# Optimization experiments

Hardware: AMD Instinct MI355X
Metric: run time of the kernel (lower is better)

The kernel has to match this reference:

```python
import jax, jax.numpy as jnp
import numpy as np

B, N, D, K, CF = 2, 4096, 128, 32, 16
EI = 2 * D + 1  # edge_input_dim = 257 (edge_feat=0, fourier_feat=0)


def setup_inputs() -> dict:
    key = jax.random.key(0)
    ks = jax.random.split(key, 10)
    rn = lambda k, shp, s=0.05: jax.random.normal(k, shp, jnp.float32) * s
    return {
        "h": rn(ks[0], (B, N, D), 1.0),
        "x": rn(ks[1], (B, N, 3), 1.0),
        "mask": jnp.ones((B, N), dtype=bool),
        # edge_mlp: Linear(EI, 2EI) -> SiLU -> Linear(2EI, CF) -> SiLU
        "We1": rn(ks[2], (EI, 2 * EI)), "be1": jnp.zeros((2 * EI,), jnp.float32),
        "We2": rn(ks[3], (2 * EI, CF)), "be2": jnp.zeros((CF,), jnp.float32),
        # coors_mlp: Linear(CF, 4CF) -> SiLU -> Linear(4CF, 1)
        "Wc1": rn(ks[4], (CF, 4 * CF)), "bc1": jnp.zeros((4 * CF,), jnp.float32),
        "Wc2": rn(ks[5], (4 * CF, 1)), "bc2": jnp.zeros((1,), jnp.float32),
        # node_mlp: Linear(D+CF, 2D) -> SiLU -> Linear(2D, D)
        "Wn1": rn(ks[6], (D + CF, 2 * D)), "bn1": jnp.zeros((2 * D,), jnp.float32),
        "Wn2": rn(ks[7], (2 * D, D)), "bn2": jnp.zeros((D,), jnp.float32),
    }


def _forward(h, x, mask, We1, be1, We2, be2, Wc1, bc1, Wc2, bc2, Wn1, bn1, Wn2, bn2):
    silu = jax.nn.silu
    b, n, d = h.shape
    # pairwise relative coordinates and squared distances
    rel = x[:, :, None, :] - x[:, None, :, :]            # [b, n, n, 3]
    dist = jnp.sum(rel * rel, axis=-1)                   # [b, n, n]
    # top-K nearest neighbors (smallest distance)
    _, idx = jax.lax.top_k(-dist, K)                     # [b, n, K]
    rel_k = jnp.take_along_axis(rel, idx[..., None], axis=2)   # [b, n, K, 3]
    dist_k = jnp.take_along_axis(dist, idx, axis=2)[..., None]  # [b, n, K, 1]
    bidx = jnp.arange(b)[:, None, None]
    feats_j = h[bidx, idx]                               # [b, n, K, d]
    feats_i = jnp.broadcast_to(h[:, :, None, :], (b, n, K, d))
    edge_in = jnp.concatenate([feats_i, feats_j, dist_k], axis=-1)  # [b, n, K, 2d+1]
    # edge MLP
    m_ij = silu(silu(edge_in @ We1 + be1) @ We2 + be2)   # [b, n, K, CF]
    # coordinate weights
    cw = (silu(m_ij @ Wc1 + bc1) @ Wc2 + bc2)[..., 0]    # [b, n, K]
    mask_ij = mask[:, :, None] & mask[bidx, idx]         # [b, n, K]
    cw = jnp.where(mask_ij, cw, 0.0)
    coors_out = jnp.einsum('bij,bijc->bic', cw, rel_k) + x
    # node update
    m_i = m_ij.sum(axis=-2)                              # [b, n, CF]
    node_in = jnp.concatenate([h, m_i], axis=-1)
    node_out = silu(node_in @ Wn1 + bn1) @ Wn2 + bn2 + h
    return node_out, coors_out


def reference(h, x, mask, We1, be1, We2, be2, Wc1, bc1, Wc2, bc2, Wn1, bn1, Wn2, bn2):
    return _forward(h, x, mask, We1, be1, We2, be2, Wc1, bc1, Wc2, bc2, Wn1, bn1, Wn2, bn2)
```

## Files before the change

kernel.cpp:

```cpp
#include <hip/hip_runtime.h>
#include <hip/hip_bf16.h>

#define BB    2
#define NNODE 4096
#define DD    128
#define KK    32
#define CFX   16

typedef __attribute__((ext_vector_type(8))) short bf16x8;
typedef __attribute__((ext_vector_type(4))) float f32x4;

__device__ __forceinline__ unsigned short f2bf(float f) {
    __hip_bfloat16 h = __float2bfloat16(f);
    return *reinterpret_cast<unsigned short*>(&h);
}
__device__ __forceinline__ unsigned pk2(float lo, float hi) {
    __hip_bfloat162 v = __float22bfloat162_rn(make_float2(lo, hi));
    return *reinterpret_cast<unsigned*>(&v);
}
__device__ __forceinline__ float silu_f(float v) {
    float e = __expf(-v);
    return v * __builtin_amdgcn_rcpf(1.f + e);
}
__device__ __forceinline__ float dist3(float xi0, float xi1, float xi2,
                                       const float* __restrict__ xb, int j) {
    float d0 = __fsub_rn(xi0, xb[3 * j]);
    float d1 = __fsub_rn(xi1, xb[3 * j + 1]);
    float d2 = __fsub_rn(xi2, xb[3 * j + 2]);
    return __fadd_rn(__fadd_rn(__fmul_rn(d0, d0), __fmul_rn(d1, d1)), __fmul_rn(d2, d2));
}

__global__ void prep_kernel(const float* __restrict__ We1, const float* __restrict__ We2,
                            const float* __restrict__ Wn1, const float* __restrict__ Wn2,
                            unsigned short* __restrict__ W1pack, unsigned short* __restrict__ W2p2,
                            unsigned short* __restrict__ Wn1p, unsigned short* __restrict__ Wn2p) {
    int tid = blockIdx.x * 256 + threadIdx.x;
    int stride = gridDim.x * 256;
    for (int p = tid; p < 9 * 36 * 64 * 8; p += stride) {
        int i = p & 7, lane = (p >> 3) & 63, rest = p >> 9;
        int nb = rest % 36, ks = rest / 36;
        int n = nb * 16 + (lane & 15);
        int k = ks * 32 + 8 * (lane >> 4) + i;
        W1pack[p] = (k < 257 && n < 514) ? f2bf(We1[k * 514 + n]) : (unsigned short)0;
    }
    for (int p = tid; p < 4 * 5 * 64 * 8; p += stride) {
        int i = p & 7, lane = (p >> 3) & 63, rest = p >> 9;
        int ks2 = rest % 5, wn = rest / 5;
        int g = lane >> 4, f = lane & 15;
        int nloc = ks2 * 32 + 16 * (i >> 2) + 4 * g + (i & 3);
        int ng = wn * 144 + nloc;
        W2p2[p] = (nloc < 144 && ng < 514) ? f2bf(We2[ng * 16 + f]) : (unsigned short)0;
    }
    for (int p = tid; p < 5 * 16 * 64 * 8; p += stride) {
        int i = p & 7, lane = (p >> 3) & 63, rest = p >> 9;
        int nb = rest % 16, ks = rest / 16;
        int u = nb * 16 + (lane & 15);
        int k = ks * 32 + 8 * (lane >> 4) + i;
        Wn1p[p] = (k < 144) ? f2bf(Wn1[k * 256 + u]) : (unsigned short)0;
    }
    for (int p = tid; p < 8 * 8 * 64 * 8; p += stride) {
        int i = p & 7, lane = (p >> 3) & 63, rest = p >> 9;
        int nb = rest % 8, ks = rest / 8;
        int d = nb * 16 + (lane & 15);
        int k = ks * 32 + 8 * (lane >> 4) + i;
        Wn2p[p] = f2bf(Wn2[k * 128 + d]);
    }
}

__global__ __launch_bounds__(256) void pre_kernel(
    const float* __restrict__ h, const float* __restrict__ be1,
    const unsigned short* __restrict__ W1pack, float* __restrict__ pre_g)
{
    __shared__ unsigned short nin[16][136];
    const int t = threadIdx.x;
    const int gn0 = blockIdx.x * 16;
    const int wn = t >> 6, lane = t & 63;
    const int l15 = lane & 15, g = lane >> 4;

    for (int q = t; q < 16 * 32; q += 256) {
        int node = q >> 5, c4 = q & 31;
        float4 v = *(const float4*)(h + (size_t)(gn0 + node) * DD + c4 * 4);
        *(uint2*)&nin[node][c4 * 4] = make_uint2(pk2(v.x, v.y), pk2(v.z, v.w));
    }
    __syncthreads();

    const bf16x8* W1v = (const bf16x8*)W1pack;
    f32x4 acc[9];
    #pragma unroll
    for (int nb = 0; nb < 9; ++nb)
        #pragma unroll
        for (int r = 0; r < 4; ++r) acc[nb][r] = 0.f;
    #pragma unroll
    for (int ks = 0; ks < 4; ++ks) {
        bf16x8 bfr = *(const bf16x8*)&nin[l15][ks * 32 + 8 * g];
        #pragma unroll
        for (int nb = 0; nb < 9; ++nb) {
            bf16x8 af = W1v[((size_t)(ks * 36 + wn * 9 + nb)) * 64 + lane];
            acc[nb] = __builtin_amdgcn_mfma_f32_16x16x32_bf16(af, bfr, acc[nb], 0, 0, 0);
        }
    }
    float* outp = pre_g + (size_t)(gn0 + l15) * 576;
    #pragma unroll
    for (int nb = 0; nb < 9; ++nb) {
        int n0 = wn * 144 + nb * 16 + 4 * g;
        float4 o;
        o.x = acc[nb][0] + ((n0 + 0) < 514 ? be1[n0 + 0] : 0.f);
        o.y = acc[nb][1] + ((n0 + 1) < 514 ? be1[n0 + 1] : 0.f);
        o.z = acc[nb][2] + ((n0 + 2) < 514 ? be1[n0 + 2] : 0.f);
        o.w = acc[nb][3] + ((n0 + 3) < 514 ? be1[n0 + 3] : 0.f);
        *(float4*)(outp + n0) = o;
    }
}

#define EQCAP 36
#define CANDCAP 1024
__global__ __launch_bounds__(256) void knn_kernel(const float* __restrict__ x,
                                                  int* __restrict__ idx_o,
                                                  float* __restrict__ relk_o,
                                                  float* __restrict__ distk_o) {
    __shared__ unsigned hist[4][256];
    __shared__ unsigned wsum[4];
    __shared__ unsigned sel[2];
    __shared__ unsigned shA, shB;
    __shared__ int out_j[KK];
    __shared__ int eqbuf[EQCAP];
    __shared__ uint2 cand[CANDCAP];

    const int t = threadIdx.x;
    const int ln = t & 63, wv = t >> 6;
    const int gn = blockIdx.x;
    const int b = gn >> 12, i = gn & 4095;
    const float* xb = x + (size_t)b * NNODE * 3;
    const float xi0 = xb[3 * i], xi1 = xb[3 * i + 1], xi2 = xb[3 * i + 2];

    #pragma unroll
    for (int q2 = 0; q2 < 4; ++q2) hist[q2][t] = 0;
    __syncthreads();

    unsigned ub[16];
    #pragma unroll
    for (int s = 0; s < 16; ++s) {
        float d = dist3(xi0, xi1, xi2, xb, t + 256 * s);
        ub[s] = __float_as_uint(d);
        atomicAdd(&hist[wv][ub[s] >> 24], 1u);
    }
    __syncthreads();

    int kk = KK;
    {
        unsigned hv = hist[0][t] + hist[1][t] + hist[2][t] + hist[3][t];
        unsigned v = hv;
        #pragma unroll
        for (int off = 1; off < 64; off <<= 1) {
            unsigned o = __shfl_up(v, off, 64);
            if (ln >= off) v += o;
        }
        if (ln == 63) wsum[wv] = v;
        __syncthreads();
        unsigned add = 0;
        #pragma unroll
        for (int w = 0; w < 4; ++w) add += (w < wv) ? wsum[w] : 0u;
        unsigned incl = v + add, excl = incl - hv;
        if ((unsigned)kk > excl && (unsigned)kk <= incl) { sel[0] = (unsigned)t; sel[1] = (unsigned)kk - excl; }
        __syncthreads();
    }
    unsigned prefix = sel[0];
    kk = (int)sel[1];
    __syncthreads();

    unsigned pc = 0;
    #pragma unroll
    for (int s = 0; s < 16; ++s) {
        unsigned tb = ub[s] >> 24;
        pc += (tb < prefix) ? 0x10000u : (tb == prefix ? 1u : 0u);
    }
    {
        unsigned v = pc;
        #pragma unroll
        for (int off = 1; off < 64; off <<= 1) {
            unsigned o = __shfl_up(v, off, 64);
            if (ln >= off) v += o;
        }
        if (ln == 63) wsum[wv] = v;
        __syncthreads();
        unsigned add = 0;
        #pragma unroll
        for (int w = 0; w < 4; ++w) add += (w < wv) ? wsum[w] : 0u;
        unsigned incl = v + add, excl = incl - pc;
        if (t == 255) { shA = incl >> 16; shB = incl & 0xFFFFu; }
        __syncthreads();
        unsigned wl = excl >> 16, wc = excl & 0xFFFFu;
        #pragma unroll
        for (int s = 0; s < 16; ++s) {
            unsigned u = ub[s];
            unsigned tb = u >> 24;
            int j = t + 256 * s;
            if (tb < prefix) { out_j[wl++] = j; }
            else if (tb == prefix) { if (wc < CANDCAP) cand[wc] = make_uint2(u, (unsigned)j); ++wc; }
        }
    }
    __syncthreads();
    const unsigned totL0 = shA, totC = shB;
    const bool fullscan = (totC > CANDCAP);

    for (int r = 1; r < 4; ++r) {
        const int sh = 24 - 8 * r;
        #pragma unroll
        for (int q2 = 0; q2 < 4; ++q2) hist[q2][t] = 0;
        __syncthreads();
        if (!fullscan) {
            for (int ii = t; ii < (int)totC; ii += 256) {
                unsigned u = cand[ii].x;
                if ((u >> (sh + 8)) == prefix) atomicAdd(&hist[wv][(u >> sh) & 255], 1u);
            }
        } else {
            #pragma unroll
            for (int s = 0; s < 16; ++s) {
                unsigned u = ub[s];
                if ((u >> (sh + 8)) == prefix) atomicAdd(&hist[wv][(u >> sh) & 255], 1u);
            }
        }
        __syncthreads();
        unsigned hv = hist[0][t] + hist[1][t] + hist[2][t] + hist[3][t];
        unsigned v = hv;
        #pragma unroll
        for (int off = 1; off < 64; off <<= 1) {
            unsigned o = __shfl_up(v, off, 64);
            if (ln >= off) v += o;
        }
        if (ln == 63) wsum[wv] = v;
        __syncthreads();
        unsigned add = 0;
        #pragma unroll
        for (int w = 0; w < 4; ++w) add += (w < wv) ? wsum[w] : 0u;
        unsigned incl = v + add, excl = incl - hv;
        if ((unsigned)kk > excl && (unsigned)kk <= incl) { sel[0] = (unsigned)t; sel[1] = (unsigned)kk - excl; }
        __syncthreads();
        prefix = (prefix << 8) | sel[0];
        kk = (int)sel[1];
        __syncthreads();
    }
    const unsigned T = prefix;

    int totL;
    if (!fullscan) {
        unsigned pc2 = 0;
        for (int ii = t; ii < (int)totC; ii += 256) {
            unsigned u = cand[ii].x;
            pc2 += (u < T) ? 0x10000u : (u == T ? 1u : 0u);
        }
        unsigned v = pc2;
        #pragma unroll
        for (int off = 1; off < 64; off <<= 1) {
            unsigned o = __shfl_up(v, off, 64);
            if (ln >= off) v += o;
        }
        if (ln == 63) wsum[wv] = v;
        __syncthreads();
        unsigned add = 0;
        #pragma unroll
        for (int w = 0; w < 4; ++w) add += (w < wv) ? wsum[w] : 0u;
        unsigned incl = v + add, excl = incl - pc2;
        if (t == 255) { shA = incl >> 16; shB = incl & 0xFFFFu; }
        __syncthreads();
        unsigned w2 = totL0 + (excl >> 16), we = excl & 0xFFFFu;
        for (int ii = t; ii < (int)totC; ii += 256) {
            unsigned u = cand[ii].x;
            int j = (int)cand[ii].y;
            if (u < T) { out_j[w2++] = j; }
            else if (u == T) { if (we < EQCAP) eqbuf[we] = j; ++we; }
        }
        __syncthreads();
        totL = (int)(totL0 + shA);
        const unsigned totE = shB;
        if (t == 0) {
            int need = KK - totL;
            if (totE <= EQCAP) {
                for (int a = 1; a < (int)totE; ++a) {
                    int key = eqbuf[a], c = a - 1;
                    while (c >= 0 && eqbuf[c] > key) { eqbuf[c + 1] = eqbuf[c]; --c; }
                    eqbuf[c + 1] = key;
                }
                for (int q = 0; q < need; ++q) out_j[totL + q] = eqbuf[q];
            } else {
                int taken = 0;
                for (int j = 0; j < NNODE && taken < need; ++j)
                    if (__float_as_uint(dist3(xi0, xi1, xi2, xb, j)) == T) out_j[totL + taken++] = j;
            }
        }
    } else {
        unsigned pc2 = 0;
        #pragma unroll
        for (int s = 0; s < 16; ++s) {
            unsigned u = ub[s];
            pc2 += (u < T) ? 0x10000u : (u == T ? 1u : 0u);
        }
        unsigned v = pc2;
        #pragma unroll
        for (int off = 1; off < 64; off <<= 1) {
            unsigned o = __shfl_up(v, off, 64);
            if (ln >= off) v += o;
        }
        if (ln == 63) wsum[wv] = v;
        __syncthreads();
        unsigned add = 0;
        #pragma unroll
        for (int w = 0; w < 4; ++w) add += (w < wv) ? wsum[w] : 0u;
        unsigned incl = v + add, excl = incl - pc2;
        if (t == 255) { shA = incl >> 16; shB = incl & 0xFFFFu; }
        __syncthreads();
        unsigned w2 = excl >> 16, we = excl & 0xFFFFu;
        #pragma unroll
        for (int s = 0; s < 16; ++s) {
            unsigned u = ub[s];
            int j = t + 256 * s;
            if (u < T) { out_j[w2++] = j; }
            else if (u == T) { if (we < EQCAP) eqbuf[we] = j; ++we; }
        }
        __syncthreads();
        totL = (int)shA;
        const unsigned totE = shB;
        if (t == 0) {
            int need = KK - totL;
            if (totE <= EQCAP) {
                for (int a = 1; a < (int)totE; ++a) {
                    int key = eqbuf[a], c = a - 1;
                    while (c >= 0 && eqbuf[c] > key) { eqbuf[c + 1] = eqbuf[c]; --c; }
                    eqbuf[c + 1] = key;
                }
                for (int q = 0; q < need; ++q) out_j[totL + q] = eqbuf[q];
            } else {
                int taken = 0;
                for (int j = 0; j < NNODE && taken < need; ++j)
                    if (__float_as_uint(dist3(xi0, xi1, xi2, xb, j)) == T) out_j[totL + taken++] = j;
            }
        }
    }
    __syncthreads();

    if (t < KK) {
        int j = out_j[t];
        size_t eo = (size_t)gn * KK + t;
        idx_o[eo] = j;
        float r0 = __fsub_rn(xi0, xb[3 * j]);
        float r1 = __fsub_rn(xi1, xb[3 * j + 1]);
        float r2 = __fsub_rn(xi2, xb[3 * j + 2]);
        relk_o[eo * 3 + 0] = r0;
        relk_o[eo * 3 + 1] = r1;
        relk_o[eo * 3 + 2] = r2;
        distk_o[eo] = __fadd_rn(__fadd_rn(__fmul_rn(r0, r0), __fmul_rn(r1, r1)), __fmul_rn(r2, r2));
    }
}

__global__ __launch_bounds__(256, 2) void edge_kernel(
    const float* __restrict__ h, const float* __restrict__ x, const int* __restrict__ mask,
    const float* __restrict__ be2,
    const float* __restrict__ Wc1, const float* __restrict__ bc1,
    const float* __restrict__ Wc2, const float* __restrict__ bc2,
    const int* __restrict__ idx, const float* __restrict__ relk, const float* __restrict__ distk,
    const unsigned short* __restrict__ W1pack, const unsigned short* __restrict__ W2p2,
    const float* __restrict__ pre_g,
    float* __restrict__ m_i_out, float* __restrict__ coors_out)
{
    __shared__ unsigned short E2[64][168];
    __shared__ float pre_s[2 * 576];
    __shared__ int   j_s[64];
    __shared__ float cw_s[64];
    __shared__ float m_s4[4 * 64 * 16];
    __shared__ float m_sF[64 * 17];

    const int t = threadIdx.x;
    const int gn0 = blockIdx.x * 2;
    const int b = gn0 >> 12;
    const int wn = t >> 6, lane = t & 63;
    const int l15 = lane & 15, g = lane >> 4;

    if (t < 64) {
        size_t eo = (size_t)gn0 * KK + t;
        j_s[t] = idx[eo];
        float dv = distk[eo];
        ushort2* p = (ushort2*)&E2[t][128];
        p[0] = make_ushort2(f2bf(dv), 0);
        #pragma unroll
        for (int z = 1; z < 20; ++z) p[z] = make_ushort2(0, 0);
    }
    {
        const float4* src = (const float4*)(pre_g + (size_t)gn0 * 576);
        float4* dst = (float4*)pre_s;
        for (int i2 = t; i2 < 288; i2 += 256) dst[i2] = src[i2];
    }
    __syncthreads();

    for (int q = t; q < 64 * 32; q += 256) {
        int e = q >> 5, d4 = q & 31;
        int j = j_s[e];
        float4 v = *(const float4*)(h + ((size_t)b * NNODE + j) * DD + d4 * 4);
        *(uint2*)&E2[e][d4 * 4] = make_uint2(pk2(v.x, v.y), pk2(v.z, v.w));
    }
    __syncthreads();

    const bf16x8* W1v = (const bf16x8*)W1pack;
    const bf16x8* W2v = (const bf16x8*)W2p2;
    int erow[4];
    #pragma unroll
    for (int et = 0; et < 4; ++et) erow[et] = et * 16 + l15;

    f32x4 acc2[4];
    #pragma unroll
    for (int et = 0; et < 4; ++et)
        #pragma unroll
        for (int r = 0; r < 4; ++r) acc2[et][r] = 0.f;

    #pragma unroll
    for (int c = 0; c < 2; ++c) {
        f32x4 acc[4][4];
        #pragma unroll
        for (int nb = 0; nb < 4; ++nb)
            #pragma unroll
            for (int et = 0; et < 4; ++et)
                acc[nb][et] = *(const f32x4*)&pre_s[(et >> 1) * 576 + wn * 144 + (c * 4 + nb) * 16 + 4 * g];
        #pragma unroll
        for (int ks = 0; ks < 5; ++ks) {
            const bf16x8* wp = W1v + ((size_t)((ks + 4) * 36 + wn * 9 + c * 4)) * 64 + lane;
            bf16x8 afr[4];
            #pragma unroll
            for (int nb = 0; nb < 4; ++nb) afr[nb] = wp[nb * 64];
            bf16x8 bfr[4];
            #pragma unroll
            for (int et = 0; et < 4; ++et)
                bfr[et] = *(const bf16x8*)&E2[erow[et]][ks * 32 + 8 * g];
            #pragma unroll
            for (int nb = 0; nb < 4; ++nb)
                #pragma unroll
                for (int et = 0; et < 4; ++et)
                    acc[nb][et] = __builtin_amdgcn_mfma_f32_16x16x32_bf16(afr[nb], bfr[et], acc[nb][et], 0, 0, 0);
        }
        #pragma unroll
        for (int nb = 0; nb < 4; ++nb)
            #pragma unroll
            for (int et = 0; et < 4; ++et)
                #pragma unroll
                for (int r = 0; r < 4; ++r)
                    acc[nb][et][r] = silu_f(acc[nb][et][r]);
        #pragma unroll
        for (int qq = 0; qq < 2; ++qq) {
            int ks2 = 2 * c + qq;
            bf16x8 a2 = W2v[(size_t)(wn * 5 + ks2) * 64 + lane];
            #pragma unroll
            for (int et = 0; et < 4; ++et) {
                union { unsigned u[4]; bf16x8 v; } cv;
                cv.u[0] = pk2(acc[2 * qq][et][0], acc[2 * qq][et][1]);
                cv.u[1] = pk2(acc[2 * qq][et][2], acc[2 * qq][et][3]);
                cv.u[2] = pk2(acc[2 * qq + 1][et][0], acc[2 * qq + 1][et][1]);
                cv.u[3] = pk2(acc[2 * qq + 1][et][2], acc[2 * qq + 1][et][3]);
                acc2[et] = __builtin_amdgcn_mfma_f32_16x16x32_bf16(a2, cv.v, acc2[et], 0, 0, 0);
            }
        }
    }
    {
        f32x4 acc8[4];
        #pragma unroll
        for (int et = 0; et < 4; ++et)
            acc8[et] = *(const f32x4*)&pre_s[(et >> 1) * 576 + wn * 144 + 128 + 4 * g];
        #pragma unroll
        for (int ks = 0; ks < 5; ++ks) {
            bf16x8 af = W1v[((size_t)((ks + 4) * 36 + wn * 9 + 8)) * 64 + lane];
            bf16x8 bfr[4];
            #pragma unroll
            for (int et = 0; et < 4; ++et)
                bfr[et] = *(const bf16x8*)&E2[erow[et]][ks * 32 + 8 * g];
            #pragma unroll
            for (int et = 0; et < 4; ++et)
                acc8[et] = __builtin_amdgcn_mfma_f32_16x16x32_bf16(af, bfr[et], acc8[et], 0, 0, 0);
        }
        #pragma unroll
        for (int et = 0; et < 4; ++et)
            #pragma unroll
            for (int r = 0; r < 4; ++r)
                acc8[et][r] = silu_f(acc8[et][r]);
        bf16x8 a2 = W2v[(size_t)(wn * 5 + 4) * 64 + lane];
        #pragma unroll
        for (int et = 0; et < 4; ++et) {
            union { unsigned u[4]; bf16x8 v; } cv;
            cv.u[0] = pk2(acc8[et][0], acc8[et][1]);
            cv.u[1] = pk2(acc8[et][2], acc8[et][3]);
            cv.u[2] = 0; cv.u[3] = 0;
            acc2[et] = __builtin_amdgcn_mfma_f32_16x16x32_bf16(a2, cv.v, acc2[et], 0, 0, 0);
        }
    }
    #pragma unroll
    for (int et = 0; et < 4; ++et)
        *(f32x4*)&m_s4[((wn * 64) + erow[et]) * 16 + 4 * g] = acc2[et];
    __syncthreads();

    #pragma unroll
    for (int i2 = t; i2 < 64 * 16; i2 += 256) {
        int e = i2 >> 4, f = i2 & 15;
        float s = m_s4[e * 16 + f] + m_s4[(64 + e) * 16 + f]
                + m_s4[(128 + e) * 16 + f] + m_s4[(192 + e) * 16 + f];
        m_sF[e * 17 + f] = silu_f(s + be2[f]);
    }
    __syncthreads();

    {
        const int ee = t >> 2, q4 = t & 3;
        const int u0 = q4 * 16;
        float mm[16];
        #pragma unroll
        for (int f = 0; f < 16; ++f) mm[f] = m_sF[ee * 17 + f];
        float h2[16];
        {
            const float4* bp = (const float4*)(bc1 + u0);
            float4 b0 = bp[0], b1 = bp[1], b2v = bp[2], b3 = bp[3];
            h2[0]=b0.x; h2[1]=b0.y; h2[2]=b0.z; h2[3]=b0.w;
            h2[4]=b1.x; h2[5]=b1.y; h2[6]=b1.z; h2[7]=b1.w;
            h2[8]=b2v.x; h2[9]=b2v.y; h2[10]=b2v.z; h2[11]=b2v.w;
            h2[12]=b3.x; h2[13]=b3.y; h2[14]=b3.z; h2[15]=b3.w;
        }
        #pragma unroll
        for (int f = 0; f < 16; ++f) {
            const float4* wp = (const float4*)(Wc1 + (size_t)f * 64 + u0);
            float4 w0 = wp[0], w1 = wp[1], w2 = wp[2], w3 = wp[3];
            float v = mm[f];
            h2[0]  = fmaf(v, w0.x, h2[0]);  h2[1]  = fmaf(v, w0.y, h2[1]);
            h2[2]  = fmaf(v, w0.z, h2[2]);  h2[3]  = fmaf(v, w0.w, h2[3]);
            h2[4]  = fmaf(v, w1.x, h2[4]);  h2[5]  = fmaf(v, w1.y, h2[5]);
            h2[6]  = fmaf(v, w1.z, h2[6]);  h2[7]  = fmaf(v, w1.w, h2[7]);
            h2[8]  = fmaf(v, w2.x, h2[8]);  h2[9]  = fmaf(v, w2.y, h2[9]);
            h2[10] = fmaf(v, w2.z, h2[10]); h2[11] = fmaf(v, w2.w, h2[11]);
            h2[12] = fmaf(v, w3.x, h2[12]); h2[13] = fmaf(v, w3.y, h2[13]);
            h2[14] = fmaf(v, w3.z, h2[14]); h2[15] = fmaf(v, w3.w, h2[15]);
        }
        float cw = 0.f;
        const float4* cp = (const float4*)(Wc2 + u0);
        float4 c0 = cp[0], c1 = cp[1], c2 = cp[2], c3 = cp[3];
        const float wv[16] = {c0.x,c0.y,c0.z,c0.w, c1.x,c1.y,c1.z,c1.w,
                              c2.x,c2.y,c2.z,c2.w, c3.x,c3.y,c3.z,c3.w};
        #pragma unroll
        for (int r = 0; r < 16; ++r) cw = fmaf(silu_f(h2[r]), wv[r], cw);
        cw += __shfl_xor(cw, 1, 64);
        cw += __shfl_xor(cw, 2, 64);
        if (q4 == 0) {
            cw += bc2[0];
            int gnode = gn0 + (ee >> 5);
            int mi = mask[gnode];
            int mj = mask[b * NNODE + j_s[ee]];
            cw_s[ee] = (mi != 0 && mj != 0) ? cw : 0.f;
        }
    }
    __syncthreads();

    if (t < 32) {
        int n = t >> 4, f = t & 15;
        float s = 0.f;
        #pragma unroll
        for (int k2 = 0; k2 < 32; ++k2) s += m_sF[(n * 32 + k2) * 17 + f];
        m_i_out[(size_t)(gn0 + n) * CFX + f] = s;
    } else if (t < 38) {
        int r = t - 32;
        int n = r / 3, c = r - n * 3;
        const float* rp = relk + ((size_t)gn0 * KK + n * 32) * 3 + c;
        float s = 0.f;
        #pragma unroll
        for (int k2 = 0; k2 < 32; ++k2) s = fmaf(cw_s[n * 32 + k2], rp[k2 * 3], s);
        coors_out[(size_t)(gn0 + n) * 3 + c] = s + x[(size_t)(gn0 + n) * 3 + c];
    }
}

__global__ __launch_bounds__(256) void node_kernel(
    const float* __restrict__ h, const float* __restrict__ m_i,
    const unsigned short* __restrict__ Wn1p, const float* __restrict__ bn1,
    const unsigned short* __restrict__ Wn2p, const float* __restrict__ bn2,
    float* __restrict__ node_out)
{
    __shared__ unsigned short nin[32][168];
    __shared__ unsigned short hid[32][264];

    const int t = threadIdx.x;
    const int gn0 = blockIdx.x * 32;
    const int wn = t >> 6, lane = t & 63;
    const int l15 = lane & 15, g = lane >> 4;

    for (int q = t; q < 32 * 32; q += 256) {
        int node = q >> 5, c4 = q & 31;
        float4 v = *(const float4*)(h + (size_t)(gn0 + node) * DD + c4 * 4);
        *(uint2*)&nin[node][c4 * 4] = make_uint2(pk2(v.x, v.y), pk2(v.z, v.w));
    }
    if (t < 128) {
        int node = t >> 2, c4 = t & 3;
        float4 v = *(const float4*)(m_i + (size_t)(gn0 + node) * CFX + c4 * 4);
        *(uint2*)&nin[node][128 + c4 * 4] = make_uint2(pk2(v.x, v.y), pk2(v.z, v.w));
    } else if (t < 224) {
        int r = t - 128;
        int node = r / 3, cc = (r - node * 3) * 8;
        *(uint4*)&nin[node][144 + cc] = make_uint4(0, 0, 0, 0);
    }
    __syncthreads();

    const bf16x8* A1 = (const bf16x8*)Wn1p;
    f32x4 acc[4][2];
    #pragma unroll
    for (int nb = 0; nb < 4; ++nb)
        #pragma unroll
        for (int et = 0; et < 2; ++et)
            #pragma unroll
            for (int r = 0; r < 4; ++r) acc[nb][et][r] = 0.f;
    #pragma unroll
    for (int ks = 0; ks < 5; ++ks) {
        const bf16x8* wp = A1 + ((size_t)(ks * 16 + wn * 4)) * 64 + lane;
        bf16x8 afr[4];
        #pragma unroll
        for (int nb = 0; nb < 4; ++nb) afr[nb] = wp[nb * 64];
        bf16x8 b0 = *(const bf16x8*)&nin[l15][ks * 32 + 8 * g];
        bf16x8 b1 = *(const bf16x8*)&nin[16 + l15][ks * 32 + 8 * g];
        #pragma unroll
        for (int nb = 0; nb < 4; ++nb) {
            acc[nb][0] = __builtin_amdgcn_mfma_f32_16x16x32_bf16(afr[nb], b0, acc[nb][0], 0, 0, 0);
            acc[nb][1] = __builtin_amdgcn_mfma_f32_16x16x32_bf16(afr[nb], b1, acc[nb][1], 0, 0, 0);
        }
    }
    #pragma unroll
    for (int nb = 0; nb < 4; ++nb) {
        int u0 = (wn * 4 + nb) * 16 + 4 * g;
        f32x4 bv = *(const f32x4*)&bn1[u0];
        #pragma unroll
        for (int et = 0; et < 2; ++et) {
            float s0 = silu_f(acc[nb][et][0] + bv[0]);
            float s1 = silu_f(acc[nb][et][1] + bv[1]);
            float s2 = silu_f(acc[nb][et][2] + bv[2]);
            float s3 = silu_f(acc[nb][et][3] + bv[3]);
            *(uint2*)&hid[et * 16 + l15][u0] = make_uint2(pk2(s0, s1), pk2(s2, s3));
        }
    }
    __syncthreads();

    const bf16x8* A2 = (const bf16x8*)Wn2p;
    f32x4 acc2[2][2];
    #pragma unroll
    for (int nb = 0; nb < 2; ++nb)
        #pragma unroll
        for (int et = 0; et < 2; ++et)
            #pragma unroll
            for (int r = 0; r < 4; ++r) acc2[nb][et][r] = 0.f;
    #pragma unroll
    for (int ks = 0; ks < 8; ++ks) {
        const bf16x8* wp = A2 + ((size_t)(ks * 8 + wn * 2)) * 64 + lane;
        bf16x8 a0 = wp[0], a1 = wp[64];
        bf16x8 b0 = *(const bf16x8*)&hid[l15][ks * 32 + 8 * g];
        bf16x8 b1 = *(const bf16x8*)&hid[16 + l15][ks * 32 + 8 * g];
        acc2[0][0] = __builtin_amdgcn_mfma_f32_16x16x32_bf16(a0, b0, acc2[0][0], 0, 0, 0);
        acc2[0][1] = __builtin_amdgcn_mfma_f32_16x16x32_bf16(a0, b1, acc2[0][1], 0, 0, 0);
        acc2[1][0] = __builtin_amdgcn_mfma_f32_16x16x32_bf16(a1, b0, acc2[1][0], 0, 0, 0);
        acc2[1][1] = __builtin_amdgcn_mfma_f32_16x16x32_bf16(a1, b1, acc2[1][1], 0, 0, 0);
    }
    #pragma unroll
    for (int nb = 0; nb < 2; ++nb) {
        int d0 = (wn * 2 + nb) * 16 + 4 * g;
        f32x4 bv = *(const f32x4*)&bn2[d0];
        #pragma unroll
        for (int et = 0; et < 2; ++et) {
            int gnode = gn0 + et * 16 + l15;
            float4 hv = *(const float4*)(h + (size_t)gnode * DD + d0);
            float4 o;
            o.x = acc2[nb][et][0] + bv[0] + hv.x;
            o.y = acc2[nb][et][1] + bv[1] + hv.y;
            o.z = acc2[nb][et][2] + bv[2] + hv.z;
            o.w = acc2[nb][et][3] + bv[3] + hv.w;
            *(float4*)(node_out + (size_t)gnode * DD + d0) = o;
        }
    }
}

extern "C" void kernel_launch(void* const* d_in, const int* in_sizes, int n_in,
                              void* d_out, int out_size, void* d_ws, size_t ws_size,
                              hipStream_t stream) {
    const float* h   = (const float*)d_in[0];
    const float* x   = (const float*)d_in[1];
    const int*   mask= (const int*)d_in[2];
    const float* We1 = (const float*)d_in[3];
    const float* be1 = (const float*)d_in[4];
    const float* We2 = (const float*)d_in[5];
    const float* be2 = (const float*)d_in[6];
    const float* Wc1 = (const float*)d_in[7];
    const float* bc1 = (const float*)d_in[8];
    const float* Wc2 = (const float*)d_in[9];
    const float* bc2 = (const float*)d_in[10];
    const float* Wn1 = (const float*)d_in[11];
    const float* bn1 = (const float*)d_in[12];
    const float* Wn2 = (const float*)d_in[13];
    const float* bn2 = (const float*)d_in[14];

    float* node_out  = (float*)d_out;
    float* coors_out = node_out + (size_t)BB * NNODE * DD;

    char* ws = (char*)d_ws;
    int*   idx    = (int*)ws;            ws += (size_t)BB * NNODE * KK * 4;
    float* relk   = (float*)ws;          ws += (size_t)BB * NNODE * KK * 3 * 4;
    float* distk  = (float*)ws;          ws += (size_t)BB * NNODE * KK * 4;
    float* m_i    = (float*)ws;          ws += (size_t)BB * NNODE * CFX * 4;
    unsigned short* W1pack = (unsigned short*)ws;  ws += (size_t)9 * 36 * 64 * 8 * 2;
    unsigned short* W2p2   = (unsigned short*)ws;  ws += (size_t)4 * 5 * 64 * 8 * 2;
    unsigned short* Wn1p   = (unsigned short*)ws;  ws += (size_t)5 * 16 * 64 * 8 * 2;
    unsigned short* Wn2p   = (unsigned short*)ws;  ws += (size_t)8 * 8 * 64 * 8 * 2;
    float* pre_g  = (float*)ws;          ws += (size_t)BB * NNODE * 576 * 4;

    prep_kernel<<<256, 256, 0, stream>>>(We1, We2, Wn1, Wn2, W1pack, W2p2, Wn1p, Wn2p);
    pre_kernel<<<BB * NNODE / 16, 256, 0, stream>>>(h, be1, W1pack, pre_g);
    knn_kernel<<<BB * NNODE, 256, 0, stream>>>(x, idx, relk, distk);
    edge_kernel<<<BB * NNODE / 2, 256, 0, stream>>>(h, x, mask, be2, Wc1, bc1, Wc2, bc2,
                                                    idx, relk, distk, W1pack, W2p2, pre_g,
                                                    m_i, coors_out);
    node_kernel<<<BB * NNODE / 32, 256, 0, stream>>>(h, m_i, Wn1p, bn1, Wn2p, bn2, node_out);
}
```

Before: 288.0 us.

## Precompute per-node neighbor projection of first edge layer, gather instead of MMA

```diff
diff --git a/kernel.cpp b/kernel.cpp
--- a/kernel.cpp
+++ b/kernel.cpp
@@ -69,7 +69,8 @@
 
 __global__ __launch_bounds__(256) void pre_kernel(
     const float* __restrict__ h, const float* __restrict__ be1,
-    const unsigned short* __restrict__ W1pack, float* __restrict__ pre_g)
+    const unsigned short* __restrict__ W1pack,
+    float* __restrict__ preI_g, unsigned short* __restrict__ preJ_g)
 {
     __shared__ unsigned short nin[16][136];
     const int t = threadIdx.x;
@@ -85,30 +86,54 @@
     __syncthreads();
 
     const bf16x8* W1v = (const bf16x8*)W1pack;
-    f32x4 acc[9];
-    #pragma unroll
-    for (int nb = 0; nb < 9; ++nb)
-        #pragma unroll
-        for (int r = 0; r < 4; ++r) acc[nb][r] = 0.f;
-    #pragma unroll
-    for (int ks = 0; ks < 4; ++ks) {
-        bf16x8 bfr = *(const bf16x8*)&nin[l15][ks * 32 + 8 * g];
+    {
+        f32x4 acc[9];
+        #pragma unroll
+        for (int nb = 0; nb < 9; ++nb)
+            #pragma unroll
+            for (int r = 0; r < 4; ++r) acc[nb][r] = 0.f;
+        #pragma unroll
+        for (int ks = 0; ks < 4; ++ks) {
+            bf16x8 bfr = *(const bf16x8*)&nin[l15][ks * 32 + 8 * g];
+            #pragma unroll
+            for (int nb = 0; nb < 9; ++nb) {
+                bf16x8 af = W1v[((size_t)(ks * 36 + wn * 9 + nb)) * 64 + lane];
+                acc[nb] = __builtin_amdgcn_mfma_f32_16x16x32_bf16(af, bfr, acc[nb], 0, 0, 0);
+            }
+        }
+        float* outp = preI_g + (size_t)(gn0 + l15) * 576;
         #pragma unroll
         for (int nb = 0; nb < 9; ++nb) {
-            bf16x8 af = W1v[((size_t)(ks * 36 + wn * 9 + nb)) * 64 + lane];
-            acc[nb] = __builtin_amdgcn_mfma_f32_16x16x32_bf16(af, bfr, acc[nb], 0, 0, 0);
-        }
-    }
-    float* outp = pre_g + (size_t)(gn0 + l15) * 576;
-    #pragma unroll
-    for (int nb = 0; nb < 9; ++nb) {
-        int n0 = wn * 144 + nb * 16 + 4 * g;
-        float4 o;
-        o.x = acc[nb][0] + ((n0 + 0) < 514 ? be1[n0 + 0] : 0.f);
-        o.y = acc[nb][1] + ((n0 + 1) < 514 ? be1[n0 + 1] : 0.f);
-        o.z = acc[nb][2] + ((n0 + 2) < 514 ? be1[n0 + 2] : 0.f);
-        o.w = acc[nb][3] + ((n0 + 3) < 514 ? be1[n0 + 3] : 0.f);
-        *(float4*)(outp + n0) = o;
+            int n0 = wn * 144 + nb * 16 + 4 * g;
+            float4 o;
+            o.x = acc[nb][0] + ((n0 + 0) < 514 ? be1[n0 + 0] : 0.f);
+            o.y = acc[nb][1] + ((n0 + 1) < 514 ? be1[n0 + 1] : 0.f);
+            o.z = acc[nb][2] + ((n0 + 2) < 514 ? be1[n0 + 2] : 0.f);
+            o.w = acc[nb][3] + ((n0 + 3) < 514 ? be1[n0 + 3] : 0.f);
+            *(float4*)(outp + n0) = o;
+        }
+    }
+    {
+        f32x4 acc[9];
+        #pragma unroll
+        for (int nb = 0; nb < 9; ++nb)
+            #pragma unroll
+            for (int r = 0; r < 4; ++r) acc[nb][r] = 0.f;
+        #pragma unroll
+        for (int ks = 0; ks < 4; ++ks) {
+            bf16x8 bfr = *(const bf16x8*)&nin[l15][ks * 32 + 8 * g];
+            #pragma unroll
+            for (int nb = 0; nb < 9; ++nb) {
+                bf16x8 af = W1v[((size_t)((ks + 4) * 36 + wn * 9 + nb)) * 64 + lane];
+                acc[nb] = __builtin_amdgcn_mfma_f32_16x16x32_bf16(af, bfr, acc[nb], 0, 0, 0);
+            }
+        }
+        unsigned short* outp = preJ_g + (size_t)(gn0 + l15) * 576;
+        #pragma unroll
+        for (int nb = 0; nb < 9; ++nb) {
+            int n0 = wn * 144 + nb * 16 + 4 * g;
+            *(uint2*)(outp + n0) = make_uint2(pk2(acc[nb][0], acc[nb][1]), pk2(acc[nb][2], acc[nb][3]));
+        }
     }
 }
 
@@ -352,19 +377,20 @@
     }
 }
 
-__global__ __launch_bounds__(256, 2) void edge_kernel(
-    const float* __restrict__ h, const float* __restrict__ x, const int* __restrict__ mask,
-    const float* __restrict__ be2,
+__global__ __launch_bounds__(256) void edge_kernel(
+    const float* __restrict__ x, const int* __restrict__ mask,
+    const float* __restrict__ We1, const float* __restrict__ be2,
     const float* __restrict__ Wc1, const float* __restrict__ bc1,
     const float* __restrict__ Wc2, const float* __restrict__ bc2,
     const int* __restrict__ idx, const float* __restrict__ relk, const float* __restrict__ distk,
-    const unsigned short* __restrict__ W1pack, const unsigned short* __restrict__ W2p2,
-    const float* __restrict__ pre_g,
+    const unsigned short* __restrict__ W2p2,
+    const float* __restrict__ preI_g, const unsigned short* __restrict__ preJ_g,
     float* __restrict__ m_i_out, float* __restrict__ coors_out)
 {
-    __shared__ unsigned short E2[64][168];
     __shared__ float pre_s[2 * 576];
+    __shared__ float wd_s[576];
     __shared__ int   j_s[64];
+    __shared__ float dist_s[64];
     __shared__ float cw_s[64];
     __shared__ float m_s4[4 * 64 * 16];
     __shared__ float m_sF[64 * 17];
@@ -378,32 +404,26 @@
     if (t < 64) {
         size_t eo = (size_t)gn0 * KK + t;
         j_s[t] = idx[eo];
-        float dv = distk[eo];
-        ushort2* p = (ushort2*)&E2[t][128];
-        p[0] = make_ushort2(f2bf(dv), 0);
-        #pragma unroll
-        for (int z = 1; z < 20; ++z) p[z] = make_ushort2(0, 0);
-    }
+        dist_s[t] = distk[eo];
+    }
+    for (int i2 = t; i2 < 576; i2 += 256) wd_s[i2] = (i2 < 514) ? We1[256 * 514 + i2] : 0.f;
     {
-        const float4* src = (const float4*)(pre_g + (size_t)gn0 * 576);
+        const float4* src = (const float4*)(preI_g + (size_t)gn0 * 576);
         float4* dst = (float4*)pre_s;
         for (int i2 = t; i2 < 288; i2 += 256) dst[i2] = src[i2];
     }
     __syncthreads();
 
-    for (int q = t; q < 64 * 32; q += 256) {
-        int e = q >> 5, d4 = q & 31;
-        int j = j_s[e];
-        float4 v = *(const float4*)(h + ((size_t)b * NNODE + j) * DD + d4 * 4);
-        *(uint2*)&E2[e][d4 * 4] = make_uint2(pk2(v.x, v.y), pk2(v.z, v.w));
-    }
-    __syncthreads();
-
-    const bf16x8* W1v = (const bf16x8*)W1pack;
     const bf16x8* W2v = (const bf16x8*)W2p2;
     int erow[4];
-    #pragma unroll
-    for (int et = 0; et < 4; ++et) erow[et] = et * 16 + l15;
+    size_t jrow[4];
+    float de[4];
+    #pragma unroll
+    for (int et = 0; et < 4; ++et) {
+        erow[et] = et * 16 + l15;
+        jrow[et] = ((size_t)b * NNODE + j_s[erow[et]]) * 576;
+        de[et] = dist_s[erow[et]];
+    }
 
     f32x4 acc2[4];
     #pragma unroll
@@ -415,33 +435,23 @@
     for (int c = 0; c < 2; ++c) {
         f32x4 acc[4][4];
         #pragma unroll
-        for (int nb = 0; nb < 4; ++nb)
-            #pragma unroll
-            for (int et = 0; et < 4; ++et)
-                acc[nb][et] = *(const f32x4*)&pre_s[(et >> 1) * 576 + wn * 144 + (c * 4 + nb) * 16 + 4 * g];
-        #pragma unroll
-        for (int ks = 0; ks < 5; ++ks) {
-            const bf16x8* wp = W1v + ((size_t)((ks + 4) * 36 + wn * 9 + c * 4)) * 64 + lane;
-            bf16x8 afr[4];
-            #pragma unroll
-            for (int nb = 0; nb < 4; ++nb) afr[nb] = wp[nb * 64];
-            bf16x8 bfr[4];
-            #pragma unroll
-            for (int et = 0; et < 4; ++et)
-                bfr[et] = *(const bf16x8*)&E2[erow[et]][ks * 32 + 8 * g];
-            #pragma unroll
-            for (int nb = 0; nb < 4; ++nb)
-                #pragma unroll
-                for (int et = 0; et < 4; ++et)
-                    acc[nb][et] = __builtin_amdgcn_mfma_f32_16x16x32_bf16(afr[nb], bfr[et], acc[nb][et], 0, 0, 0);
-        }
-        #pragma unroll
-        for (int nb = 0; nb < 4; ++nb)
-            #pragma unroll
-            for (int et = 0; et < 4; ++et)
-                #pragma unroll
-                for (int r = 0; r < 4; ++r)
-                    acc[nb][et][r] = silu_f(acc[nb][et][r]);
+        for (int nb = 0; nb < 4; ++nb) {
+            const int n0 = wn * 144 + (c * 4 + nb) * 16 + 4 * g;
+            f32x4 wdv = *(const f32x4*)&wd_s[n0];
+            #pragma unroll
+            for (int et = 0; et < 4; ++et) {
+                f32x4 pi = *(const f32x4*)&pre_s[(et >> 1) * 576 + n0];
+                uint2 pj = *(const uint2*)(preJ_g + jrow[et] + n0);
+                float p0 = __uint_as_float(pj.x << 16);
+                float p1 = __uint_as_float(pj.x & 0xFFFF0000u);
+                float p2 = __uint_as_float(pj.y << 16);
+                float p3 = __uint_as_float(pj.y & 0xFFFF0000u);
+                acc[nb][et][0] = silu_f(pi[0] + p0 + de[et] * wdv[0]);
+                acc[nb][et][1] = silu_f(pi[1] + p1 + de[et] * wdv[1]);
+                acc[nb][et][2] = silu_f(pi[2] + p2 + de[et] * wdv[2]);
+                acc[nb][et][3] = silu_f(pi[3] + p3 + de[et] * wdv[3]);
+            }
+        }
         #pragma unroll
         for (int qq = 0; qq < 2; ++qq) {
             int ks2 = 2 * c + qq;
@@ -459,25 +469,21 @@
     }
     {
         f32x4 acc8[4];
-        #pragma unroll
-        for (int et = 0; et < 4; ++et)
-            acc8[et] = *(const f32x4*)&pre_s[(et >> 1) * 576 + wn * 144 + 128 + 4 * g];
-        #pragma unroll
-        for (int ks = 0; ks < 5; ++ks) {
-            bf16x8 af = W1v[((size_t)((ks + 4) * 36 + wn * 9 + 8)) * 64 + lane];
-            bf16x8 bfr[4];
-            #pragma unroll
-            for (int et = 0; et < 4; ++et)
-                bfr[et] = *(const bf16x8*)&E2[erow[et]][ks * 32 + 8 * g];
-            #pragma unroll
-            for (int et = 0; et < 4; ++et)
-                acc8[et] = __builtin_amdgcn_mfma_f32_16x16x32_bf16(af, bfr[et], acc8[et], 0, 0, 0);
-        }
-        #pragma unroll
-        for (int et = 0; et < 4; ++et)
-            #pragma unroll
-            for (int r = 0; r < 4; ++r)
-                acc8[et][r] = silu_f(acc8[et][r]);
+        const int n0 = wn * 144 + 128 + 4 * g;
+        f32x4 wdv = *(const f32x4*)&wd_s[n0];
+        #pragma unroll
+        for (int et = 0; et < 4; ++et) {
+            f32x4 pi = *(const f32x4*)&pre_s[(et >> 1) * 576 + n0];
+            uint2 pj = *(const uint2*)(preJ_g + jrow[et] + n0);
+            float p0 = __uint_as_float(pj.x << 16);
+            float p1 = __uint_as_float(pj.x & 0xFFFF0000u);
+            float p2 = __uint_as_float(pj.y << 16);
+            float p3 = __uint_as_float(pj.y & 0xFFFF0000u);
+            acc8[et][0] = silu_f(pi[0] + p0 + de[et] * wdv[0]);
+            acc8[et][1] = silu_f(pi[1] + p1 + de[et] * wdv[1]);
+            acc8[et][2] = silu_f(pi[2] + p2 + de[et] * wdv[2]);
+            acc8[et][3] = silu_f(pi[3] + p3 + de[et] * wdv[3]);
+        }
         bf16x8 a2 = W2v[(size_t)(wn * 5 + 4) * 64 + lane];
         #pragma unroll
         for (int et = 0; et < 4; ++et) {
@@ -702,13 +708,14 @@
     unsigned short* W2p2   = (unsigned short*)ws;  ws += (size_t)4 * 5 * 64 * 8 * 2;
     unsigned short* Wn1p   = (unsigned short*)ws;  ws += (size_t)5 * 16 * 64 * 8 * 2;
     unsigned short* Wn2p   = (unsigned short*)ws;  ws += (size_t)8 * 8 * 64 * 8 * 2;
-    float* pre_g  = (float*)ws;          ws += (size_t)BB * NNODE * 576 * 4;
+    float* preI_g = (float*)ws;          ws += (size_t)BB * NNODE * 576 * 4;
+    unsigned short* preJ_g = (unsigned short*)ws;  ws += (size_t)BB * NNODE * 576 * 2;
 
     prep_kernel<<<256, 256, 0, stream>>>(We1, We2, Wn1, Wn2, W1pack, W2p2, Wn1p, Wn2p);
-    pre_kernel<<<BB * NNODE / 16, 256, 0, stream>>>(h, be1, W1pack, pre_g);
+    pre_kernel<<<BB * NNODE / 16, 256, 0, stream>>>(h, be1, W1pack, preI_g, preJ_g);
     knn_kernel<<<BB * NNODE, 256, 0, stream>>>(x, idx, relk, distk);
-    edge_kernel<<<BB * NNODE / 2, 256, 0, stream>>>(h, x, mask, be2, Wc1, bc1, Wc2, bc2,
-                                                    idx, relk, distk, W1pack, W2p2, pre_g,
+    edge_kernel<<<BB * NNODE / 2, 256, 0, stream>>>(x, mask, We1, be2, Wc1, bc1, Wc2, bc2,
+                                                    idx, relk, distk, W2p2, preI_g, preJ_g,
                                                     m_i, coors_out);
     node_kernel<<<BB * NNODE / 32, 256, 0, stream>>>(h, m_i, Wn1p, bn1, Wn2p, bn2, node_out);
 }
```

New measurement: 275.1 us, median of 2. 4.5% less time.
